# Performance work log

Hardware: AMD Instinct MI355X
Metric: run time of the kernel (lower is better)

## Reference

```python
import jax, jax.numpy as jnp
import numpy as np

N_NODES, N_LAYERS, D = 4096, 8, 128


def setup_inputs() -> dict:
    key = jax.random.key(0)
    k1, k2, k3 = jax.random.split(key, 3)
    feature = jax.random.normal(k1, (N_NODES, N_LAYERS, D), dtype=jnp.float32)
    W = jax.random.uniform(k2, (D, D), dtype=jnp.float32)
    adj = jax.random.randint(k3, (N_LAYERS, N_NODES, N_NODES), 0, 2, dtype=jnp.int32)
    return {"feature": feature, "W": W, "adj": adj}


def reference(feature, W, adj):
    # feature: [N, L, D]; W: [D, D]; adj: [L, N, N] with 0/1 entries.
    # Original loop: for i, for l, for j in neighbors(i) U {i}:
    #     ret[j, l, :] = (W @ feature[i, l, :]) / sqrt(d_i * d_j)   # OVERWRITE
    # => final ret[j, l] uses the LAST source i with adj[l,i,j]==1 or i==j.
    L, N = adj.shape[0], adj.shape[1]
    i_idx = jnp.arange(N)
    # mask[l, i, j]: source i writes to destination j at layer l
    mask = (adj == 1) | (i_idx[:, None] == i_idx[None, :])
    # last (largest) source index per (l, j); diagonal guarantees >= 0
    src = jnp.max(jnp.where(mask, i_idx[:, None], -1), axis=1)          # [L, N]
    deg = jnp.sum(adj, axis=2).astype(feature.dtype) + 1.0              # [L, N]
    # shared tiny GEMM applied to all (node, layer) features
    Wf = jnp.einsum('de,nle->lnd', W, feature)                          # [L, N, D]
    gathered = jnp.take_along_axis(Wf, src[:, :, None], axis=1)         # [L, N, D]
    d_src = jnp.take_along_axis(deg, src, axis=1)                       # [L, N]
    scale = 1.0 / jnp.sqrt(d_src * deg)                                 # [L, N]
    ret = jnp.transpose(gathered * scale[:, :, None], (1, 0, 2))        # [N, L, D]
    return ret
```

## Files before the change

### kernel.cpp

```cpp
#include <hip/hip_runtime.h>
#include <cstddef>

#define NN 4096
#define NL 8
#define ND 128

#define SRC_BLOCKS (NL * (NN / 256))

typedef int   int4v   __attribute__((ext_vector_type(4)));
typedef float float4v __attribute__((ext_vector_type(4)));


__global__ __launch_bounds__(256) void degsrc_kernel(const int* __restrict__ adj,
                                                     float* __restrict__ deg,
                                                     int* __restrict__ src,
                                                     unsigned* __restrict__ used) {
  __shared__ unsigned lmask[128];
  __shared__ int ws[4];

  if (blockIdx.x < SRC_BLOCKS) {
    const int bid = blockIdx.x;
    const int l = bid >> 4;
    const int j = ((bid & 15) << 8) + threadIdx.x;
    const int* __restrict__ A = adj + (size_t)l * NN * NN + j;
    if (threadIdx.x < 128) lmask[threadIdx.x] = 0u;
    __syncthreads();
    int cur = j;
    bool found = false;
    int itop = NN - 1;
    while (true) {
      int ibot = itop - 31;
      if (ibot < 0) ibot = 0;
      int best = -1;
#pragma unroll
      for (int k = 0; k < 32; ++k) {
        int i = itop - k;
        int a = (i >= ibot) ? A[(size_t)i * NN] : 0;
        int c = (a != 0 && i > j) ? i : -1;
        if (c > best) best = c;
      }
      if (!found && best >= 0) { cur = best; found = true; }
      bool done = found || (ibot <= j + 1);
      if (__syncthreads_and((int)done)) break;
      itop = ibot - 1;
    }
    src[l * NN + j] = cur;
    atomicOr(&lmask[cur >> 5], 1u << (cur & 31));
    __syncthreads();
    if (threadIdx.x < 128) used[bid * 128 + threadIdx.x] = lmask[threadIdx.x];
  } else {
    const size_t row2 = (size_t)(blockIdx.x - SRC_BLOCKS) * 2;
    const int r = threadIdx.x >> 7;
    const int t = threadIdx.x & 127;
    const int4v* __restrict__ p =
        reinterpret_cast<const int4v*>(adj + (row2 + r) * (size_t)NN);
    int s = 0;
#pragma unroll
    for (int k = 0; k < 8; ++k) {
      int4v v = __builtin_nontemporal_load(&p[t + k * 128]);
      s += v.x + v.y + v.z + v.w;
    }
    for (int off = 32; off > 0; off >>= 1) s += __shfl_down(s, off, 64);
    if ((threadIdx.x & 63) == 0) ws[threadIdx.x >> 6] = s;
    __syncthreads();
    if (threadIdx.x == 0)   deg[row2]     = (float)(ws[0] + ws[1]) + 1.0f;
    if (threadIdx.x == 128) deg[row2 + 1] = (float)(ws[2] + ws[3]) + 1.0f;
  }
}

__global__ __launch_bounds__(128) void wf_kernel(const float* __restrict__ feature,
                                                 const float* __restrict__ W,
                                                 const unsigned* __restrict__ used,
                                                 float* __restrict__ Wf) {
  const int i = blockIdx.x;
  const int l = blockIdx.y;
  const int w = i >> 5;
  const unsigned bit = 1u << (i & 31);
  unsigned m = 0;
#pragma unroll
  for (int c = 0; c < 16; ++c) m |= used[(l * 16 + c) * 128 + w];
  if (!(m & bit)) return;

  __shared__ float fbuf[ND];
  if (threadIdx.x < 32)
    reinterpret_cast<float4v*>(fbuf)[threadIdx.x] =
        reinterpret_cast<const float4v*>(feature + ((size_t)i * NL + l) * ND)[threadIdx.x];
  __syncthreads();

  const int d = threadIdx.x;
  float acc = 0.0f;
#pragma unroll 8
  for (int eq = 0; eq < 32; ++eq) {
    float4v wv = reinterpret_cast<const float4v*>(W + (size_t)d * ND)[eq];
    float4v fv = reinterpret_cast<const float4v*>(fbuf)[eq];
    acc += wv.x * fv.x + wv.y * fv.y + wv.z * fv.z + wv.w * fv.w;
  }
  Wf[((size_t)l * NN + i) * ND + d] = acc;
}

__global__ __launch_bounds__(256) void out_kernel(const float* __restrict__ Wf,
                                                  const float* __restrict__ deg,
                                                  const int* __restrict__ src,
                                                  float* __restrict__ out) {
  const int g = blockIdx.x * 256 + threadIdx.x;
  const int q = g & 31;
  const int jl = g >> 5;
  const int l = jl & 7;
  const int j = jl >> 3;
  const int s = src[l * NN + j];
  const float sc = rsqrtf(deg[l * NN + s] * deg[l * NN + j]);
  float4v v = reinterpret_cast<const float4v*>(Wf + ((size_t)l * NN + s) * ND)[q];
  v.x *= sc; v.y *= sc; v.z *= sc; v.w *= sc;
  __builtin_nontemporal_store(v, reinterpret_cast<float4v*>(out) + g);
}

extern "C" void kernel_launch(void* const* d_in, const int* in_sizes, int n_in,
                              void* d_out, int out_size, void* d_ws,
                              size_t ws_size, hipStream_t stream) {
  const float* feature = (const float*)d_in[0];
  const float* W       = (const float*)d_in[1];
  const int*   adj     = (const int*)d_in[2];
  float* out = (float*)d_out;

  char* ws = (char*)d_ws;
  float*    deg  = (float*)(ws);
  int*      src  = (int*)(ws + 131072);
  unsigned* used = (unsigned*)(ws + 262144);
  float*    Wf   = (float*)(ws + 327680);

  degsrc_kernel<<<SRC_BLOCKS + NL * NN / 2, 256, 0, stream>>>(adj, deg, src, used);
  wf_kernel<<<dim3(NN, NL), 128, 0, stream>>>(feature, W, used, Wf);
  out_kernel<<<NN * NL * ND / 4 / 256, 256, 0, stream>>>(Wf, deg, src, out);
}
```

Baseline: 108.4 us.

## Compact used source nodes into worklist and run persistent Wf kernel over it

```diff
diff --git a/kernel.cpp b/kernel.cpp
--- a/kernel.cpp
+++ b/kernel.cpp
@@ -6,6 +6,8 @@
 #define ND 128
 
 #define SRC_BLOCKS (NL * (NN / 256))
+#define ROWS 4
+#define WF_BLOCKS 256
 
 typedef int   int4v   __attribute__((ext_vector_type(4)));
 typedef float float4v __attribute__((ext_vector_type(4)));
@@ -13,18 +15,12 @@
 
 __global__ __launch_bounds__(256) void degsrc_kernel(const int* __restrict__ adj,
                                                      float* __restrict__ deg,
-                                                     int* __restrict__ src,
-                                                     unsigned* __restrict__ used) {
-  __shared__ unsigned lmask[128];
-  __shared__ int ws[4];
-
+                                                     int* __restrict__ src) {
   if (blockIdx.x < SRC_BLOCKS) {
     const int bid = blockIdx.x;
     const int l = bid >> 4;
     const int j = ((bid & 15) << 8) + threadIdx.x;
     const int* __restrict__ A = adj + (size_t)l * NN * NN + j;
-    if (threadIdx.x < 128) lmask[threadIdx.x] = 0u;
-    __syncthreads();
     int cur = j;
     bool found = false;
     int itop = NN - 1;
@@ -45,57 +41,85 @@
       itop = ibot - 1;
     }
     src[l * NN + j] = cur;
-    atomicOr(&lmask[cur >> 5], 1u << (cur & 31));
-    __syncthreads();
-    if (threadIdx.x < 128) used[bid * 128 + threadIdx.x] = lmask[threadIdx.x];
   } else {
-    const size_t row2 = (size_t)(blockIdx.x - SRC_BLOCKS) * 2;
-    const int r = threadIdx.x >> 7;
-    const int t = threadIdx.x & 127;
+    const size_t row = (size_t)(blockIdx.x - SRC_BLOCKS) * ROWS +
+                       (threadIdx.x >> 6);
+    const int lane = threadIdx.x & 63;
     const int4v* __restrict__ p =
-        reinterpret_cast<const int4v*>(adj + (row2 + r) * (size_t)NN);
+        reinterpret_cast<const int4v*>(adj + row * (size_t)NN);
     int s = 0;
 #pragma unroll
-    for (int k = 0; k < 8; ++k) {
-      int4v v = __builtin_nontemporal_load(&p[t + k * 128]);
+    for (int k = 0; k < 16; ++k) {
+      int4v v = __builtin_nontemporal_load(&p[lane + k * 64]);
       s += v.x + v.y + v.z + v.w;
     }
     for (int off = 32; off > 0; off >>= 1) s += __shfl_down(s, off, 64);
-    if ((threadIdx.x & 63) == 0) ws[threadIdx.x >> 6] = s;
-    __syncthreads();
-    if (threadIdx.x == 0)   deg[row2]     = (float)(ws[0] + ws[1]) + 1.0f;
-    if (threadIdx.x == 128) deg[row2 + 1] = (float)(ws[2] + ws[3]) + 1.0f;
+    if (lane == 0) deg[row] = (float)s + 1.0f;
   }
+}
+
+__global__ __launch_bounds__(256) void compact_kernel(const int* __restrict__ src,
+                                                      int* __restrict__ wl,
+                                                      int* __restrict__ count) {
+  const int l = blockIdx.x;
+  __shared__ unsigned mask[NN / 32];
+  __shared__ int cnt;
+  if (threadIdx.x < NN / 32) mask[threadIdx.x] = 0u;
+  if (threadIdx.x == 0) cnt = 0;
+  __syncthreads();
+  for (int k = threadIdx.x; k < NN; k += 256) {
+    int s = src[l * NN + k];
+    atomicOr(&mask[s >> 5], 1u << (s & 31));
+  }
+  __syncthreads();
+  if (threadIdx.x < NN / 32) {
+    unsigned m = mask[threadIdx.x];
+    while (m) {
+      int b = __ffs(m) - 1;
+      m &= m - 1;
+      int pos = atomicAdd(&cnt, 1);
+      wl[l * NN + pos] = (threadIdx.x << 5) | b;
+    }
+  }
+  __syncthreads();
+  if (threadIdx.x == 0) count[l] = cnt;
 }
 
 __global__ __launch_bounds__(128) void wf_kernel(const float* __restrict__ feature,
                                                  const float* __restrict__ W,
-                                                 const unsigned* __restrict__ used,
+                                                 const int* __restrict__ wl,
+                                                 const int* __restrict__ count,
                                                  float* __restrict__ Wf) {
-  const int i = blockIdx.x;
-  const int l = blockIdx.y;
-  const int w = i >> 5;
-  const unsigned bit = 1u << (i & 31);
-  unsigned m = 0;
-#pragma unroll
-  for (int c = 0; c < 16; ++c) m |= used[(l * 16 + c) * 128 + w];
-  if (!(m & bit)) return;
+  __shared__ int base[NL + 1];
+  __shared__ float fbuf[ND];
+  if (threadIdx.x == 0) {
+    int s = 0;
+    for (int l = 0; l < NL; ++l) { base[l] = s; s += count[l]; }
+    base[NL] = s;
+  }
+  __syncthreads();
+  const int total = base[NL];
+  const int d = threadIdx.x;
 
-  __shared__ float fbuf[ND];
-  if (threadIdx.x < 32)
-    reinterpret_cast<float4v*>(fbuf)[threadIdx.x] =
-        reinterpret_cast<const float4v*>(feature + ((size_t)i * NL + l) * ND)[threadIdx.x];
-  __syncthreads();
-
-  const int d = threadIdx.x;
-  float acc = 0.0f;
+  for (int t = blockIdx.x; t < total; t += WF_BLOCKS) {
+    int l = 0;
+    while (t >= base[l + 1]) ++l;
+    const int i = wl[l * NN + (t - base[l])];
+    if (threadIdx.x < 32)
+      reinterpret_cast<float4v*>(fbuf)[threadIdx.x] =
+          reinterpret_cast<const float4v*>(
+              feature + ((size_t)i * NL + l) * ND)[threadIdx.x];
+    __syncthreads();
+    float acc = 0.0f;
 #pragma unroll 8
-  for (int eq = 0; eq < 32; ++eq) {
-    float4v wv = reinterpret_cast<const float4v*>(W + (size_t)d * ND)[eq];
-    float4v fv = reinterpret_cast<const float4v*>(fbuf)[eq];
-    acc += wv.x * fv.x + wv.y * fv.y + wv.z * fv.z + wv.w * fv.w;
+    for (int eq = 0; eq < 32; ++eq) {
+      float4v wv = reinterpret_cast<const float4v*>(W + (size_t)d * ND)[eq];
+      float4v fv = reinterpret_cast<const float4v*>(fbuf)[eq];
+      acc += wv.x * fv.x + wv.y * fv.y + wv.z * fv.z + wv.w * fv.w;
+    }
+    Wf[((size_t)l * NN + i) * ND + d] = acc;
+    __syncthreads();
   }
-  Wf[((size_t)l * NN + i) * ND + d] = acc;
 }
 
 __global__ __launch_bounds__(256) void out_kernel(const float* __restrict__ Wf,
@@ -123,12 +147,14 @@
   float* out = (float*)d_out;
 
   char* ws = (char*)d_ws;
-  float*    deg  = (float*)(ws);
-  int*      src  = (int*)(ws + 131072);
-  unsigned* used = (unsigned*)(ws + 262144);
-  float*    Wf   = (float*)(ws + 327680);
+  float* deg   = (float*)(ws);
+  int*   src   = (int*)(ws + 131072);
+  int*   wl    = (int*)(ws + 262144);
+  int*   count = (int*)(ws + 393216);
+  float* Wf    = (float*)(ws + 409600);
 
-  degsrc_kernel<<<SRC_BLOCKS + NL * NN / 2, 256, 0, stream>>>(adj, deg, src, used);
-  wf_kernel<<<dim3(NN, NL), 128, 0, stream>>>(feature, W, used, Wf);
+  degsrc_kernel<<<SRC_BLOCKS + NL * NN / ROWS, 256, 0, stream>>>(adj, deg, src);
+  compact_kernel<<<NL, 256, 0, stream>>>(src, wl, count);
+  wf_kernel<<<WF_BLOCKS, 128, 0, stream>>>(feature, W, wl, count, Wf);
   out_kernel<<<NN * NL * ND / 4 / 256, 256, 0, stream>>>(Wf, deg, src, out);
 }
```

Measured after the change: 101.4 us. -6.4%, faster.
